# Kernel optimization log

Hardware: AMD Instinct MI355X
Metric: run time of the kernel (lower is better)

## Reference

```python
import jax, jax.numpy as jnp
import numpy as np

BOX_SIZE = 120
RESOLUTION = 1.0
NUM_NEIGHBOURS = 2
NUM_TYPES = 11
MAX_ATOMS = 512
BATCH = 4


def setup_inputs() -> dict:
    key = jax.random.key(0)
    k1, k2 = jax.random.split(key)
    # coords uniformly inside the box with a margin so Gaussians stay mostly in-grid
    margin = 5.0
    input_coords = jax.random.uniform(
        k1, (BATCH, NUM_TYPES, 3 * MAX_ATOMS), dtype=jnp.float32,
        minval=margin, maxval=BOX_SIZE * RESOLUTION - margin)
    num_atoms = jax.random.randint(k2, (BATCH, NUM_TYPES), 1, MAX_ATOMS + 1).astype(jnp.int64)
    return {"input_coords": input_coords, "num_atoms": num_atoms}


def _coords2volume(input_coords, num_atoms):
    B, T, C = input_coords.shape
    A = C // 3
    pos = input_coords.reshape(B * T, A, 3)  # [BT, A, 3] xyz per atom
    n = NUM_NEIGHBOURS
    res = RESOLUTION
    # (2n+1)^3 neighbour-cell offsets
    r = jnp.arange(-n, n + 1)
    offs = jnp.stack(jnp.meshgrid(r, r, r, indexing="ij"), axis=-1).reshape(-1, 3)  # [K,3]
    # home cell of each atom (spatial hash cell)
    cell = jnp.floor(pos / res).astype(jnp.int32)  # [BT, A, 3]
    nb = cell[:, :, None, :] + offs[None, None, :, :]  # [BT, A, K, 3]
    # truncated Gaussian density at neighbour-cell grid points
    cell_pos = nb.astype(pos.dtype) * res
    r2 = jnp.sum((cell_pos - pos[:, :, None, :]) ** 2, axis=-1)  # [BT, A, K]
    val = jnp.exp(-r2 / (res * res))
    # mask cells outside the grid and padded atoms
    in_box = jnp.all((nb >= 0) & (nb < BOX_SIZE), axis=-1)  # [BT, A, K]
    atom_mask = jnp.arange(A)[None, :] < num_atoms.reshape(-1)[:, None]  # [BT, A]
    val = jnp.where(in_box & atom_mask[:, :, None], val, 0.0)
    # scatter-add into flattened voxel grid
    flat = (nb[..., 0] * BOX_SIZE + nb[..., 1]) * BOX_SIZE + nb[..., 2]
    flat = jnp.clip(flat, 0, BOX_SIZE ** 3 - 1)
    vol = jnp.zeros((B * T, BOX_SIZE ** 3), dtype=pos.dtype)
    bidx = jnp.arange(B * T)[:, None, None]
    vol = vol.at[bidx, flat].add(val)
    return vol.reshape(B, T, BOX_SIZE, BOX_SIZE, BOX_SIZE)


def reference(input_coords, num_atoms):
    return _coords2volume(input_coords, num_atoms)
```

## Files before the change

### kernel.cpp

```cpp
#include <hip/hip_runtime.h>

#define BOX 120
#define BOX3 (BOX * BOX * BOX)
#define NTYPES 11
#define NBATCH 4
#define BT (NBATCH * NTYPES)
#define MAXA 512
#define NNB 2
#define KCELLS 125

__global__ __launch_bounds__(256)
void TypedCoords2Volume_scatter(const float* __restrict__ coords,
                                const int* __restrict__ num_atoms,
                                float* __restrict__ out) {
    int idx = blockIdx.x * blockDim.x + threadIdx.x;
    const int total = BT * MAXA * KCELLS;
    if (idx >= total) return;

    int k   = idx % KCELLS;
    int tmp = idx / KCELLS;
    int a   = tmp % MAXA;
    int bt  = tmp / MAXA;

    int na = num_atoms[bt];
    if (a >= na) return;

    const float* p = coords + (size_t)bt * (3 * MAXA) + (size_t)a * 3;
    float px = p[0];
    float py = p[1];
    float pz = p[2];

    int cx = (int)floorf(px);
    int cy = (int)floorf(py);
    int cz = (int)floorf(pz);

    int dz = k % 5;
    int t2 = k / 5;
    int dy = t2 % 5;
    int dx = t2 / 5;

    int nx = cx + dx - NNB;
    int ny = cy + dy - NNB;
    int nz = cz + dz - NNB;

    if ((unsigned)nx >= BOX || (unsigned)ny >= BOX || (unsigned)nz >= BOX) return;

    float fx = (float)nx - px;
    float fy = (float)ny - py;
    float fz = (float)nz - pz;
    float r2 = fx * fx + fy * fy + fz * fz;
    float val = __expf(-r2);

    size_t off = (size_t)bt * BOX3 + (size_t)((nx * BOX + ny) * BOX + nz);
    atomicAdd(out + off, val);
}

extern "C" void kernel_launch(void* const* d_in, const int* in_sizes, int n_in,
                              void* d_out, int out_size, void* d_ws, size_t ws_size,
                              hipStream_t stream) {
    const float* coords    = (const float*)d_in[0];
    const int*   num_atoms = (const int*)d_in[1];
    float*       out       = (float*)d_out;

    hipMemsetAsync(d_out, 0, (size_t)out_size, stream);

    const int total  = BT * MAXA * KCELLS;
    const int block  = 256;
    const int grid   = (total + block - 1) / block;
    TypedCoords2Volume_scatter<<<grid, block, 0, stream>>>(coords, num_atoms, out);
}
```

Baseline: 297.8 us.

## Replace atomic scatter with tiled gather writing each voxel once

Switches from per-atom atomic scatter to per-tile gather. Each block owns an 8x8 xy column tile and collects nearby atoms into shared memory. It then computes each voxel's density in registers and writes the full volume once with nontemporal stores, so no memset is needed. This removes global atomics and the separate zeroing pass. The risk is that the CAP of 64 candidates per tile could silently drop atoms in a dense tile, and blocks with no atoms still do full-tile writes.

```diff
diff --git a/kernel.cpp b/kernel.cpp
--- a/kernel.cpp
+++ b/kernel.cpp
@@ -1,58 +1,105 @@
 #include <hip/hip_runtime.h>
 
 #define BOX 120
+#define BOX2 (BOX * BOX)
 #define BOX3 (BOX * BOX * BOX)
 #define NTYPES 11
 #define NBATCH 4
 #define BT (NBATCH * NTYPES)
 #define MAXA 512
 #define NNB 2
-#define KCELLS 125
+#define TILE 8
+#define NT (BOX / TILE)
+#define CAP 64
 
-__global__ __launch_bounds__(256)
-void TypedCoords2Volume_scatter(const float* __restrict__ coords,
-                                const int* __restrict__ num_atoms,
-                                float* __restrict__ out) {
-    int idx = blockIdx.x * blockDim.x + threadIdx.x;
-    const int total = BT * MAXA * KCELLS;
-    if (idx >= total) return;
+__global__ __launch_bounds__(512)
+void TypedCoords2Volume_gather(const float* __restrict__ coords,
+                               const int* __restrict__ num_atoms,
+                               float* __restrict__ out)
+{
+    __shared__ float sx[CAP], sy[CAP], sz[CAP];
+    __shared__ int scnt;
 
-    int k   = idx % KCELLS;
-    int tmp = idx / KCELLS;
-    int a   = tmp % MAXA;
-    int bt  = tmp / MAXA;
+    const int bid = blockIdx.x;
+    const int bt  = bid / (NT * NT);
+    const int tt  = bid % (NT * NT);
+    const int x0  = (tt / NT) * TILE;
+    const int y0  = (tt % NT) * TILE;
 
-    int na = num_atoms[bt];
-    if (a >= na) return;
+    const int tid = threadIdx.x;
+    if (tid == 0) scnt = 0;
+    __syncthreads();
 
-    const float* p = coords + (size_t)bt * (3 * MAXA) + (size_t)a * 3;
-    float px = p[0];
-    float py = p[1];
-    float pz = p[2];
+    const int na = num_atoms[bt];
+    if (tid < na) {
+        const float* p = coords + (size_t)bt * (3 * MAXA) + tid * 3;
+        float px = p[0], py = p[1], pz = p[2];
+        int cx = (int)floorf(px);
+        int cy = (int)floorf(py);
+        if ((unsigned)(cx - x0 + NNB) <= (unsigned)(TILE + 2 * NNB - 1) &&
+            (unsigned)(cy - y0 + NNB) <= (unsigned)(TILE + 2 * NNB - 1)) {
+            int slot = atomicAdd(&scnt, 1);
+            if (slot < CAP) { sx[slot] = px; sy[slot] = py; sz[slot] = pz; }
+        }
+    }
+    __syncthreads();
+    const int ncand = min(scnt, CAP);
 
-    int cx = (int)floorf(px);
-    int cy = (int)floorf(py);
-    int cz = (int)floorf(pz);
+    const int wave = tid >> 6;
+    const int lane = tid & 63;
+    const int x    = x0 + wave;
+    const int z1i  = 64 + lane;
+    const float zf0 = (float)lane;
+    const float zf1 = (float)z1i;
 
-    int dz = k % 5;
-    int t2 = k / 5;
-    int dy = t2 % 5;
-    int dx = t2 / 5;
+    float acc[TILE][2];
+#pragma unroll
+    for (int y = 0; y < TILE; ++y) { acc[y][0] = 0.0f; acc[y][1] = 0.0f; }
 
-    int nx = cx + dx - NNB;
-    int ny = cy + dy - NNB;
-    int nz = cz + dz - NNB;
+    for (int ci = 0; ci < ncand; ++ci) {
+        const float px = sx[ci], py = sy[ci], pz = sz[ci];
+        const int cx = (int)floorf(px);
+        if ((unsigned)(x - cx + NNB) > 2u * NNB) continue;
+        const int cy = (int)floorf(py);
+        const int cz = (int)floorf(pz);
 
-    if ((unsigned)nx >= BOX || (unsigned)ny >= BOX || (unsigned)nz >= BOX) return;
+        const float fx  = (float)x - px;
+        const float fx2 = fx * fx;
 
-    float fx = (float)nx - px;
-    float fy = (float)ny - py;
-    float fz = (float)nz - pz;
-    float r2 = fx * fx + fy * fy + fz * fz;
-    float val = __expf(-r2);
+        const bool haveC0 = (cz - NNB <= 63);
+        const bool haveC1 = (cz + NNB >= 64);
+        const bool m0 = ((unsigned)(lane - cz + NNB) <= 2u * NNB);
+        const bool m1 = ((unsigned)(z1i  - cz + NNB) <= 2u * NNB) && (z1i < BOX);
+        const float fz0 = zf0 - pz;
+        const float fz1 = zf1 - pz;
+        const float fz0s = fz0 * fz0;
+        const float fz1s = fz1 * fz1;
 
-    size_t off = (size_t)bt * BOX3 + (size_t)((nx * BOX + ny) * BOX + nz);
-    atomicAdd(out + off, val);
+#pragma unroll
+        for (int y = 0; y < TILE; ++y) {
+            const int yy = y0 + y;
+            if ((unsigned)(yy - cy + NNB) > 2u * NNB) continue;
+            const float fy   = (float)yy - py;
+            const float fxy2 = fx2 + fy * fy;
+            if (haveC0) {
+                float v = m0 ? __expf(-(fxy2 + fz0s)) : 0.0f;
+                acc[y][0] += v;
+            }
+            if (haveC1) {
+                float v = m1 ? __expf(-(fxy2 + fz1s)) : 0.0f;
+                acc[y][1] += v;
+            }
+        }
+    }
+
+    float* base = out + (size_t)bt * BOX3 + (size_t)x * BOX2 + (size_t)y0 * BOX;
+#pragma unroll
+    for (int y = 0; y < TILE; ++y) {
+        float* row = base + y * BOX;
+        __builtin_nontemporal_store(acc[y][0], row + lane);
+        if (lane < BOX - 64)
+            __builtin_nontemporal_store(acc[y][1], row + 64 + lane);
+    }
 }
 
 extern "C" void kernel_launch(void* const* d_in, const int* in_sizes, int n_in,
@@ -62,10 +109,6 @@
     const int*   num_atoms = (const int*)d_in[1];
     float*       out       = (float*)d_out;
 
-    hipMemsetAsync(d_out, 0, (size_t)out_size, stream);
-
-    const int total  = BT * MAXA * KCELLS;
-    const int block  = 256;
-    const int grid   = (total + block - 1) / block;
-    TypedCoords2Volume_scatter<<<grid, block, 0, stream>>>(coords, num_atoms, out);
+    const int grid = BT * NT * NT;
+    TypedCoords2Volume_gather<<<grid, 512, 0, stream>>>(coords, num_atoms, out);
 }
```

Result: slower. 326.0 us (+9.5%).
